# Optimization experiments

Hardware: AMD Instinct MI355X
Metric: run time of the kernel (lower is better)

## Reference

```python
import jax, jax.numpy as jnp
from jax import lax
import numpy as np

EPS = 1e-5
NEG_SLOPE = 0.2

# 4D conv via lax.conv_general_dilated (supports arbitrary spatial rank)
_DN = ('NCABXY', 'OIABXY', 'NCABXY')  # N,C + 4 spatial dims

def conv4d(x, w):
    # x: (N, Cin, S1, S2, H, W); w: (Cout, Cin, 3, 3, 3, 3); padding=1, stride=1
    return lax.conv_general_dilated(
        x, w,
        window_strides=(1, 1, 1, 1),
        padding=[(1, 1)] * 4,
        dimension_numbers=_DN,
    )

def instance_norm4d(x):
    # normalize per (n, c) over all 4 spatial dims; no affine (PyTorch default)
    mean = jnp.mean(x, axis=(2, 3, 4, 5), keepdims=True)
    var = jnp.var(x, axis=(2, 3, 4, 5), keepdims=True)
    return (x - mean) * lax.rsqrt(var + EPS)

def leaky_relu(x):
    return jnp.where(x >= 0, x, NEG_SLOPE * x)

def setup_inputs() -> dict:
    key = jax.random.key(0)
    k0, k1, k2 = jax.random.split(key, 3)
    image = jax.random.normal(k0, (1, 16, 8, 16, 64, 64), dtype=jnp.float32)
    # He-ish init scale for kernel 3^4
    w1 = jax.random.normal(k1, (32, 16, 3, 3, 3, 3), dtype=jnp.float32) * 0.03
    w2 = jax.random.normal(k2, (32, 32, 3, 3, 3, 3), dtype=jnp.float32) * 0.02
    return {"image": image, "w1": w1, "w2": w2}

def reference(image, w1, w2):
    x = leaky_relu(instance_norm4d(conv4d(image, w1)))
    x = leaky_relu(instance_norm4d(conv4d(x, w2)))
    return x
```

## Files before the change

kernel.cpp:

```cpp
#include <hip/hip_runtime.h>

#define D1 8
#define D2 16
#define HH 64
#define WW 64
#define SPATIAL (D1*D2*HH*WW)
#define EPS 1e-5f
#define NEG 0.2f

typedef unsigned short u16;
typedef __attribute__((ext_vector_type(8))) short s16x8;
typedef __attribute__((ext_vector_type(8))) unsigned short u16x8;
typedef __attribute__((ext_vector_type(4))) unsigned short u16x4;
typedef __attribute__((ext_vector_type(4))) float f32x4;

__device__ __forceinline__ u16 f2bf(float f) {
    unsigned int u = __builtin_bit_cast(unsigned int, f);
    return (u16)((u + 0x7FFFu + ((u >> 16) & 1u)) >> 16);
}
__device__ __forceinline__ float bf2f(u16 u) {
    unsigned int v = ((unsigned int)u) << 16;
    return __builtin_bit_cast(float, v);
}
__device__ __forceinline__ float leaky(float x) {
    return x >= 0.f ? x : NEG * x;
}

__device__ __forceinline__ void decode_block(int flat, int& a, int& b, int& h0) {
    int xcd  = flat & 7;
    int slot = flat >> 3;
    int ht   = slot & 7;
    int b0   = (slot >> 3) & 1;
    a        = (slot >> 4) & 7;
    b        = xcd * 2 + b0;
    h0       = ht * 8;
}

__global__ __launch_bounds__(256)
void prep(const float* __restrict__ img, const float* __restrict__ w1,
          const float* __restrict__ w2, u16* __restrict__ imgT,
          u16* __restrict__ w1t, u16* __restrict__ w2t, float* __restrict__ st)
{
    const int bid = blockIdx.x;
    const int tid = threadIdx.x;
    if (bid < 2048) {
        int p = bid * 256 + tid;
        u16 r[16];
        #pragma unroll
        for (int c = 0; c < 16; ++c)
            r[c] = f2bf(img[(size_t)c * SPATIAL + p]);
        u16x8 lo, hi;
        #pragma unroll
        for (int j = 0; j < 8; ++j) { lo[j] = r[j]; hi[j] = r[8 + j]; }
        u16x8* dst = (u16x8*)(imgT + (size_t)p * 16);
        dst[0] = lo;
        dst[1] = hi;
    } else if (bid < 2264) {
        int i = (bid - 2048) * 256 + tid;
        if (i >= 55296) return;
        int k    = i & 31;
        int co   = (i >> 5) & 31;
        int grp  = (i >> 10) & 1;
        int rest = i >> 11;
        int dh   = rest % 3;
        int p    = rest / 3;
        int da = p / 3, db = p % 3;
        float v = 0.f;
        if (grp == 0) {
            int dw = k >> 4, ci = k & 15;
            v = w1[((((co * 16 + ci) * 3 + da) * 3 + db) * 3 + dh) * 3 + dw];
        } else if (k < 16) {
            v = w1[((((co * 16 + k) * 3 + da) * 3 + db) * 3 + dh) * 3 + 2];
        }
        w1t[i] = f2bf(v);
    } else if (bid < 2588) {
        int i = (bid - 2264) * 256 + tid;
        if (i >= 82944) return;
        int ci = i & 31;
        int co = (i >> 5) & 31;
        int t  = (i >> 10) % 9;
        int p  = (i >> 10) / 9;
        int da = p / 3, db = p % 3, dh = t / 3, dw = t % 3;
        w2t[i] = f2bf(w2[((((co * 32 + ci) * 3 + da) * 3 + db) * 3 + dh) * 3 + dw]);
    } else {
        if (tid < 128) st[tid] = 0.f;
    }
}

__global__ __launch_bounds__(256, 3)
void conv1_mfma(const u16* __restrict__ xT, const u16* __restrict__ w1t,
                u16* __restrict__ y1, float* __restrict__ st1)
{
    __shared__ __align__(16) u16 lds[660 * 24];
    __shared__ float sred[64];

    const int tid = threadIdx.x;
    int a, b, h0;
    decode_block(blockIdx.x, a, b, h0);
    const int lane = tid & 63;
    const int wv   = tid >> 6;
    const int kq   = lane >> 4;
    const int m    = lane & 15;
    const int wseg = wv << 4;

    unsigned pm = 0;
    #pragma unroll
    for (int p = 0; p < 9; ++p) {
        int ap = a + p / 3 - 1, bp = b + p % 3 - 1;
        if (ap >= 0 && ap < D1 && bp >= 0 && bp < D2) pm |= 1u << p;
    }

    const int p0 = tid >> 1, g = tid & 1;
    unsigned vmask = 0;
    int goff[6];
    #pragma unroll
    for (int k = 0; k < 6; ++k) {
        int pos = p0 + 128 * k;
        int row = pos / 66, col = pos - row * 66;
        int h = h0 - 1 + row, w = col - 1;
        bool v = (pos < 660) && col >= 1 && col <= 64 && h >= 0 && h < HH;
        goff[k] = v ? (h * WW + w) * 16 + g * 8 : 0;
        vmask |= (unsigned)v << k;
    }
    const int lbase = p0 * 24 + g * 8;

    for (int e = tid; e < 660; e += 256) {
        int row = e / 66, col = e - row * 66;
        int h = h0 - 1 + row;
        if (col == 0 || col == 65 || h < 0 || h >= HH) {
            u16x8 z = (u16x8)0;
            *(u16x8*)&lds[e * 24]     = z;
            *(u16x8*)&lds[e * 24 + 8] = z;
        }
    }

    f32x4 acc[8][2];
    #pragma unroll
    for (int i = 0; i < 8; ++i)
        #pragma unroll
        for (int nt = 0; nt < 2; ++nt)
            acc[i][nt] = (f32x4)0.f;

    int p = 0;
    while (!((pm >> p) & 1)) ++p;

    u16x8 pf[6];
    {
        int ap = a + p / 3 - 1, bp = b + p % 3 - 1;
        const u16* src = xT + (size_t)(ap * D2 + bp) * (HH * WW * 16);
        #pragma unroll
        for (int k = 0; k < 6; ++k)
            if ((vmask >> k) & 1) pf[k] = *(const u16x8*)(src + goff[k]);
    }

    while (p < 9) {
        int pn = p + 1;
        while (pn < 9 && !((pm >> pn) & 1)) ++pn;

        #pragma unroll
        for (int k = 0; k < 6; ++k)
            if ((vmask >> k) & 1) *(u16x8*)&lds[lbase + k * 3072] = pf[k];
        __syncthreads();

        const u16* srcn = nullptr;
        if (pn < 9)
            srcn = xT + (size_t)((a + pn / 3 - 1) * D2 + (b + pn % 3 - 1))
                      * (HH * WW * 16);

        const u16* wbase = w1t + p * 6144;
        #pragma unroll
        for (int grp = 0; grp < 2; ++grp) {
            s16x8 bf[3][2];
            #pragma unroll
            for (int dh = 0; dh < 3; ++dh) {
                const u16* wb = wbase + (dh * 2 + grp) * 1024;
                bf[dh][0] = *(const s16x8*)(wb + m * 32 + kq * 8);
                bf[dh][1] = *(const s16x8*)(wb + (m + 16) * 32 + kq * 8);
            }
            const int cshift = (grp == 0) ? (kq >> 1) : 2;
            const int ebase  = (kq & 1) * 8;
            #pragma unroll
            for (int x = 0; x < 10; ++x) {
                int pos = x * 66 + wseg + m + cshift;
                s16x8 af = *(const s16x8*)&lds[pos * 24 + ebase];
                #pragma unroll
                for (int dh = 0; dh < 3; ++dh) {
                    int i = x - dh;
                    if (i >= 0 && i < 8) {
                        acc[i][0] = __builtin_amdgcn_mfma_f32_16x16x32_bf16(af, bf[dh][0], acc[i][0], 0, 0, 0);
                        acc[i][1] = __builtin_amdgcn_mfma_f32_16x16x32_bf16(af, bf[dh][1], acc[i][1], 0, 0, 0);
                    }
                }
            }
            if (pn < 9) {
                #pragma unroll
                for (int k = grp * 3; k < grp * 3 + 3; ++k)
                    if ((vmask >> k) & 1) pf[k] = *(const u16x8*)(srcn + goff[k]);
            }
        }
        __syncthreads();
        p = pn;
    }

    if (tid < 64) sred[tid] = 0.f;
    __syncthreads();

    float s[2] = {0.f, 0.f}, s2[2] = {0.f, 0.f};
    const size_t plane_out = (size_t)(a * D2 + b) * (HH * WW);
    #pragma unroll
    for (int i = 0; i < 8; ++i) {
        int h  = h0 + i;
        int w0 = wseg + kq * 4;
        #pragma unroll
        for (int nt = 0; nt < 2; ++nt) {
            int co = m + nt * 16;
            #pragma unroll
            for (int reg = 0; reg < 4; ++reg) {
                float v = acc[i][nt][reg];
                s[nt]  += v;
                s2[nt] += v * v;
                y1[(plane_out + h * WW + (w0 + reg)) * 32 + co] = f2bf(v);
            }
        }
    }
    #pragma unroll
    for (int nt = 0; nt < 2; ++nt) {
        s[nt]  += __shfl_xor(s[nt], 16);  s[nt]  += __shfl_xor(s[nt], 32);
        s2[nt] += __shfl_xor(s2[nt], 16); s2[nt] += __shfl_xor(s2[nt], 32);
    }
    if (kq == 0) {
        atomicAdd(&sred[m * 2],            s[0]);
        atomicAdd(&sred[m * 2 + 1],        s2[0]);
        atomicAdd(&sred[(m + 16) * 2],     s[1]);
        atomicAdd(&sred[(m + 16) * 2 + 1], s2[1]);
    }
    __syncthreads();
    if (tid < 64) atomicAdd(&st1[tid], sred[tid]);
}

__global__ __launch_bounds__(256)
void norm1_kernel(u16* __restrict__ y1, const float* __restrict__ st1)
{
    const int tid = threadIdx.x;
    const int q   = tid & 3;
    const float invN = 1.f / (float)SPATIAL;
    float mean[8], scl[8];
    #pragma unroll
    for (int j = 0; j < 8; ++j) {
        int ci  = q * 8 + j;
        float mu = st1[ci * 2] * invN;
        float va = st1[ci * 2 + 1] * invN - mu * mu;
        mean[j] = mu;
        scl[j]  = rsqrtf(va + EPS);
    }
    #pragma unroll
    for (int j4 = 0; j4 < 4; ++j4) {
        size_t gidx = (size_t)blockIdx.x * 1024 + j4 * 256 + tid;
        u16x8* ptr = (u16x8*)(y1 + gidx * 8);
        u16x8 v = *ptr;
        u16x8 o;
        #pragma unroll
        for (int j = 0; j < 8; ++j)
            o[j] = f2bf(leaky((bf2f(v[j]) - mean[j]) * scl[j]));
        *ptr = o;
    }
}

__global__ __launch_bounds__(256, 3)
void conv2_mfma(const u16* __restrict__ y1, const u16* __restrict__ w2t,
                u16* __restrict__ y2, float* __restrict__ st2)
{
    __shared__ __align__(16) u16 lds[660 * 40];
    __shared__ float sred[64];

    const int tid = threadIdx.x;
    int a, b, h0;
    decode_block(blockIdx.x, a, b, h0);
    const int lane = tid & 63;
    const int wv   = tid >> 6;
    const int kq   = lane >> 4;
    const int m    = lane & 15;
    const int wseg = wv << 4;

    unsigned pm = 0;
    #pragma unroll
    for (int p = 0; p < 9; ++p) {
        int ap = a + p / 3 - 1, bp = b + p % 3 - 1;
        if (ap >= 0 && ap < D1 && bp >= 0 && bp < D2) pm |= 1u << p;
    }

    const int p0 = tid >> 2, q = tid & 3;
    unsigned vmask = 0;
    int goff[11];
    #pragma unroll
    for (int k = 0; k < 11; ++k) {
        int pos = p0 + 64 * k;
        int row = pos / 66, col = pos - row * 66;
        int h = h0 - 1 + row, w = col - 1;
        bool v = (pos < 660) && col >= 1 && col <= 64 && h >= 0 && h < HH;
        goff[k] = v ? (h * WW + w) * 32 + q * 8 : 0;
        vmask |= (unsigned)v << k;
    }
    const int lbase = p0 * 40 + q * 8;

    for (int e = tid; e < 660; e += 256) {
        int row = e / 66, col = e - row * 66;
        int h = h0 - 1 + row;
        if (col == 0 || col == 65 || h < 0 || h >= HH) {
            u16x8 z = (u16x8)0;
            #pragma unroll
            for (int gg = 0; gg < 4; ++gg)
                *(u16x8*)&lds[e * 40 + gg * 8] = z;
        }
    }

    f32x4 acc[8][2];
    #pragma unroll
    for (int i = 0; i < 8; ++i)
        #pragma unroll
        for (int nt = 0; nt < 2; ++nt)
            acc[i][nt] = (f32x4)0.f;

    int p = 0;
    while (!((pm >> p) & 1)) ++p;

    u16x8 pf[11];
    {
        int ap = a + p / 3 - 1, bp = b + p % 3 - 1;
        const u16* src = y1 + (size_t)(ap * D2 + bp) * (HH * WW * 32);
        #pragma unroll
        for (int k = 0; k < 11; ++k)
            if ((vmask >> k) & 1) pf[k] = *(const u16x8*)(src + goff[k]);
    }

    while (p < 9) {
        int pn = p + 1;
        while (pn < 9 && !((pm >> pn) & 1)) ++pn;

        #pragma unroll
        for (int k = 0; k < 11; ++k)
            if ((vmask >> k) & 1) *(u16x8*)&lds[lbase + k * 2560] = pf[k];
        __syncthreads();

        const u16* srcn = nullptr;
        if (pn < 9)
            srcn = y1 + (size_t)((a + pn / 3 - 1) * D2 + (b + pn % 3 - 1))
                      * (HH * WW * 32);

        const u16* wbase = w2t + p * 9216;
        #pragma unroll
        for (int dw = 0; dw < 3; ++dw) {
            s16x8 bf[3][2];
            #pragma unroll
            for (int dh = 0; dh < 3; ++dh) {
                const u16* wb = wbase + (dh * 3 + dw) * 1024;
                bf[dh][0] = *(const s16x8*)(wb + m * 32 + kq * 8);
                bf[dh][1] = *(const s16x8*)(wb + (m + 16) * 32 + kq * 8);
            }
            #pragma unroll
            for (int x = 0; x < 10; ++x) {
                int pos = x * 66 + wseg + dw + m;
                s16x8 af = *(const s16x8*)&lds[pos * 40 + kq * 8];
                #pragma unroll
                for (int dh = 0; dh < 3; ++dh) {
                    int i = x - dh;
                    if (i >= 0 && i < 8) {
                        acc[i][0] = __builtin_amdgcn_mfma_f32_16x16x32_bf16(af, bf[dh][0], acc[i][0], 0, 0, 0);
                        acc[i][1] = __builtin_amdgcn_mfma_f32_16x16x32_bf16(af, bf[dh][1], acc[i][1], 0, 0, 0);
                    }
                }
            }
            if (pn < 9) {
                const int k0 = dw * 4;
                const int k1 = (dw == 2) ? 11 : (k0 + 4);
                #pragma unroll
                for (int k = k0; k < k1; ++k)
                    if ((vmask >> k) & 1) pf[k] = *(const u16x8*)(srcn + goff[k]);
            }
        }
        __syncthreads();
        p = pn;
    }

    if (tid < 64) sred[tid] = 0.f;
    __syncthreads();

    float s[2] = {0.f, 0.f}, s2[2] = {0.f, 0.f};
    #pragma unroll
    for (int i = 0; i < 8; ++i) {
        int h  = h0 + i;
        int w0 = wseg + kq * 4;
        #pragma unroll
        for (int nt = 0; nt < 2; ++nt) {
            int co = m + nt * 16;
            u16x4 pk;
            #pragma unroll
            for (int reg = 0; reg < 4; ++reg) {
                float v = acc[i][nt][reg];
                s[nt]  += v;
                s2[nt] += v * v;
                pk[reg] = f2bf(v);
            }
            size_t off = ((size_t)(co * D1 + a) * D2 + b) * (HH * WW) + h * WW + w0;
            *(u16x4*)(y2 + off) = pk;
        }
    }
    #pragma unroll
    for (int nt = 0; nt < 2; ++nt) {
        s[nt]  += __shfl_xor(s[nt], 16);  s[nt]  += __shfl_xor(s[nt], 32);
        s2[nt] += __shfl_xor(s2[nt], 16); s2[nt] += __shfl_xor(s2[nt], 32);
    }
    if (kq == 0) {
        atomicAdd(&sred[m * 2],            s[0]);
        atomicAdd(&sred[m * 2 + 1],        s2[0]);
        atomicAdd(&sred[(m + 16) * 2],     s[1]);
        atomicAdd(&sred[(m + 16) * 2 + 1], s2[1]);
    }
    __syncthreads();
    if (tid < 64) atomicAdd(&st2[tid], sred[tid]);
}

__global__ __launch_bounds__(256)
void norm2_kernel(const u16* __restrict__ y2, const float* __restrict__ st2,
                  float* __restrict__ out)
{
    size_t i4 = (size_t)blockIdx.x * 256 + threadIdx.x;
    int c = (int)(i4 >> 17);
    const float invN = 1.f / (float)SPATIAL;
    float mu = st2[c * 2] * invN;
    float va = st2[c * 2 + 1] * invN - mu * mu;
    float sc = rsqrtf(va + EPS);
    u16x4 v = *(const u16x4*)(y2 + i4 * 4);
    float4 o;
    o.x = leaky((bf2f(v[0]) - mu) * sc);
    o.y = leaky((bf2f(v[1]) - mu) * sc);
    o.z = leaky((bf2f(v[2]) - mu) * sc);
    o.w = leaky((bf2f(v[3]) - mu) * sc);
    *(float4*)(out + i4 * 4) = o;
}

extern "C" void kernel_launch(void* const* d_in, const int* in_sizes, int n_in,
                              void* d_out, int out_size, void* d_ws, size_t ws_size,
                              hipStream_t stream)
{
    const float* image = (const float*)d_in[0];
    const float* w1    = (const float*)d_in[1];
    const float* w2    = (const float*)d_in[2];
    float* out = (float*)d_out;

    u16*   imgT = (u16*)d_ws;
    u16*   y1   = (u16*)((char*)d_ws + 33554432);
    u16*   y2   = imgT;
    float* st   = (float*)((char*)d_ws + 67108864);
    float* st1  = st;
    float* st2  = st + 64;

    u16* w1t = (u16*)((char*)d_out + 66832384);
    u16* w2t = (u16*)((char*)d_out + 66942976);

    prep<<<2589, 256, 0, stream>>>(image, w1, w2, imgT, w1t, w2t, st);

    conv1_mfma<<<1024, 256, 0, stream>>>(imgT, w1t, y1, st1);
    norm1_kernel<<<2048, 256, 0, stream>>>(y1, st1);
    conv2_mfma<<<1024, 256, 0, stream>>>(y1, w2t, y2, st2);
    norm2_kernel<<<16384, 256, 0, stream>>>(y2, st2, out);
}
```

Before: 265.9 us.

## Halve conv output tile to 8x32 and double grid for higher occupancy

Both MFMA conv kernels now compute an 8-row by 32-column output tile instead of 8x64. The four waves form a 2x2 arrangement, each computing 4 rows by 16 columns, so accumulator and prefetch registers shrink, LDS halo tiles shrink, launch bounds rise to 5 blocks per CU, and the grid doubles to 2048 blocks. The goal is more concurrent waves and better latency hiding. In exchange the halo overhead per output grows (6 rows loaded per 4 computed instead of 10 per 8, plus extra column halo), which means more LDS reads and global loads per MFMA.

```diff
diff --git a/kernel.cpp b/kernel.cpp
--- a/kernel.cpp
+++ b/kernel.cpp
@@ -26,14 +26,17 @@
     return x >= 0.f ? x : NEG * x;
 }
 
-__device__ __forceinline__ void decode_block(int flat, int& a, int& b, int& h0) {
+__device__ __forceinline__ void decode_block(int flat, int& a, int& b,
+                                             int& h0, int& w0) {
     int xcd  = flat & 7;
     int slot = flat >> 3;
     int ht   = slot & 7;
-    int b0   = (slot >> 3) & 1;
-    a        = (slot >> 4) & 7;
+    int wt   = (slot >> 3) & 1;
+    int b0   = (slot >> 4) & 1;
+    a        = (slot >> 5) & 7;
     b        = xcd * 2 + b0;
     h0       = ht * 8;
+    w0       = wt * 32;
 }
 
 __global__ __launch_bounds__(256)
@@ -87,21 +90,22 @@
     }
 }
 
-__global__ __launch_bounds__(256, 3)
+__global__ __launch_bounds__(256, 5)
 void conv1_mfma(const u16* __restrict__ xT, const u16* __restrict__ w1t,
                 u16* __restrict__ y1, float* __restrict__ st1)
 {
-    __shared__ __align__(16) u16 lds[660 * 24];
+    __shared__ __align__(16) u16 lds[340 * 24];
     __shared__ float sred[64];
 
     const int tid = threadIdx.x;
-    int a, b, h0;
-    decode_block(blockIdx.x, a, b, h0);
+    int a, b, h0, w0;
+    decode_block(blockIdx.x, a, b, h0, w0);
     const int lane = tid & 63;
     const int wv   = tid >> 6;
     const int kq   = lane >> 4;
     const int m    = lane & 15;
-    const int wseg = wv << 4;
+    const int wsl  = (wv & 1) << 4;
+    const int r0   = (wv >> 1) << 2;
 
     unsigned pm = 0;
     #pragma unroll
@@ -112,31 +116,31 @@
 
     const int p0 = tid >> 1, g = tid & 1;
     unsigned vmask = 0;
-    int goff[6];
-    #pragma unroll
-    for (int k = 0; k < 6; ++k) {
+    int goff[3];
+    #pragma unroll
+    for (int k = 0; k < 3; ++k) {
         int pos = p0 + 128 * k;
-        int row = pos / 66, col = pos - row * 66;
-        int h = h0 - 1 + row, w = col - 1;
-        bool v = (pos < 660) && col >= 1 && col <= 64 && h >= 0 && h < HH;
+        int row = pos / 34, col = pos - row * 34;
+        int h = h0 - 1 + row, w = w0 + col - 1;
+        bool v = (pos < 340) && w >= 0 && w < WW && h >= 0 && h < HH;
         goff[k] = v ? (h * WW + w) * 16 + g * 8 : 0;
         vmask |= (unsigned)v << k;
     }
     const int lbase = p0 * 24 + g * 8;
 
-    for (int e = tid; e < 660; e += 256) {
-        int row = e / 66, col = e - row * 66;
-        int h = h0 - 1 + row;
-        if (col == 0 || col == 65 || h < 0 || h >= HH) {
+    for (int e = tid; e < 340; e += 256) {
+        int row = e / 34, col = e - row * 34;
+        int h = h0 - 1 + row, w = w0 + col - 1;
+        if (w < 0 || w >= WW || h < 0 || h >= HH) {
             u16x8 z = (u16x8)0;
             *(u16x8*)&lds[e * 24]     = z;
             *(u16x8*)&lds[e * 24 + 8] = z;
         }
     }
 
-    f32x4 acc[8][2];
-    #pragma unroll
-    for (int i = 0; i < 8; ++i)
+    f32x4 acc[4][2];
+    #pragma unroll
+    for (int i = 0; i < 4; ++i)
         #pragma unroll
         for (int nt = 0; nt < 2; ++nt)
             acc[i][nt] = (f32x4)0.f;
@@ -144,12 +148,12 @@
     int p = 0;
     while (!((pm >> p) & 1)) ++p;
 
-    u16x8 pf[6];
+    u16x8 pf[3];
     {
         int ap = a + p / 3 - 1, bp = b + p % 3 - 1;
         const u16* src = xT + (size_t)(ap * D2 + bp) * (HH * WW * 16);
         #pragma unroll
-        for (int k = 0; k < 6; ++k)
+        for (int k = 0; k < 3; ++k)
             if ((vmask >> k) & 1) pf[k] = *(const u16x8*)(src + goff[k]);
     }
 
@@ -158,7 +162,7 @@
         while (pn < 9 && !((pm >> pn) & 1)) ++pn;
 
         #pragma unroll
-        for (int k = 0; k < 6; ++k)
+        for (int k = 0; k < 3; ++k)
             if ((vmask >> k) & 1) *(u16x8*)&lds[lbase + k * 3072] = pf[k];
         __syncthreads();
 
@@ -180,21 +184,22 @@
             const int cshift = (grp == 0) ? (kq >> 1) : 2;
             const int ebase  = (kq & 1) * 8;
             #pragma unroll
-            for (int x = 0; x < 10; ++x) {
-                int pos = x * 66 + wseg + m + cshift;
+            for (int xi = 0; xi < 6; ++xi) {
+                int pos = (r0 + xi) * 34 + wsl + m + cshift;
                 s16x8 af = *(const s16x8*)&lds[pos * 24 + ebase];
                 #pragma unroll
                 for (int dh = 0; dh < 3; ++dh) {
-                    int i = x - dh;
-                    if (i >= 0 && i < 8) {
+                    int i = xi - dh;
+                    if (i >= 0 && i < 4) {
                         acc[i][0] = __builtin_amdgcn_mfma_f32_16x16x32_bf16(af, bf[dh][0], acc[i][0], 0, 0, 0);
                         acc[i][1] = __builtin_amdgcn_mfma_f32_16x16x32_bf16(af, bf[dh][1], acc[i][1], 0, 0, 0);
                     }
                 }
             }
             if (pn < 9) {
+                const int k0 = grp * 1, k1 = grp ? 3 : 1;
                 #pragma unroll
-                for (int k = grp * 3; k < grp * 3 + 3; ++k)
+                for (int k = k0; k < k1; ++k)
                     if ((vmask >> k) & 1) pf[k] = *(const u16x8*)(srcn + goff[k]);
             }
         }
@@ -208,9 +213,9 @@
     float s[2] = {0.f, 0.f}, s2[2] = {0.f, 0.f};
     const size_t plane_out = (size_t)(a * D2 + b) * (HH * WW);
     #pragma unroll
-    for (int i = 0; i < 8; ++i) {
-        int h  = h0 + i;
-        int w0 = wseg + kq * 4;
+    for (int i = 0; i < 4; ++i) {
+        int h  = h0 + r0 + i;
+        int w  = w0 + wsl + kq * 4;
         #pragma unroll
         for (int nt = 0; nt < 2; ++nt) {
             int co = m + nt * 16;
@@ -219,7 +224,7 @@
                 float v = acc[i][nt][reg];
                 s[nt]  += v;
                 s2[nt] += v * v;
-                y1[(plane_out + h * WW + (w0 + reg)) * 32 + co] = f2bf(v);
+                y1[(plane_out + h * WW + (w + reg)) * 32 + co] = f2bf(v);
             }
         }
     }
@@ -266,21 +271,22 @@
     }
 }
 
-__global__ __launch_bounds__(256, 3)
+__global__ __launch_bounds__(256, 5)
 void conv2_mfma(const u16* __restrict__ y1, const u16* __restrict__ w2t,
                 u16* __restrict__ y2, float* __restrict__ st2)
 {
-    __shared__ __align__(16) u16 lds[660 * 40];
+    __shared__ __align__(16) u16 lds[340 * 40];
     __shared__ float sred[64];
 
     const int tid = threadIdx.x;
-    int a, b, h0;
-    decode_block(blockIdx.x, a, b, h0);
+    int a, b, h0, w0;
+    decode_block(blockIdx.x, a, b, h0, w0);
     const int lane = tid & 63;
     const int wv   = tid >> 6;
     const int kq   = lane >> 4;
     const int m    = lane & 15;
-    const int wseg = wv << 4;
+    const int wsl  = (wv & 1) << 4;
+    const int r0   = (wv >> 1) << 2;
 
     unsigned pm = 0;
     #pragma unroll
@@ -291,22 +297,22 @@
 
     const int p0 = tid >> 2, q = tid & 3;
     unsigned vmask = 0;
-    int goff[11];
-    #pragma unroll
-    for (int k = 0; k < 11; ++k) {
+    int goff[6];
+    #pragma unroll
+    for (int k = 0; k < 6; ++k) {
         int pos = p0 + 64 * k;
-        int row = pos / 66, col = pos - row * 66;
-        int h = h0 - 1 + row, w = col - 1;
-        bool v = (pos < 660) && col >= 1 && col <= 64 && h >= 0 && h < HH;
+        int row = pos / 34, col = pos - row * 34;
+        int h = h0 - 1 + row, w = w0 + col - 1;
+        bool v = (pos < 340) && w >= 0 && w < WW && h >= 0 && h < HH;
         goff[k] = v ? (h * WW + w) * 32 + q * 8 : 0;
         vmask |= (unsigned)v << k;
     }
     const int lbase = p0 * 40 + q * 8;
 
-    for (int e = tid; e < 660; e += 256) {
-        int row = e / 66, col = e - row * 66;
-        int h = h0 - 1 + row;
-        if (col == 0 || col == 65 || h < 0 || h >= HH) {
+    for (int e = tid; e < 340; e += 256) {
+        int row = e / 34, col = e - row * 34;
+        int h = h0 - 1 + row, w = w0 + col - 1;
+        if (w < 0 || w >= WW || h < 0 || h >= HH) {
             u16x8 z = (u16x8)0;
             #pragma unroll
             for (int gg = 0; gg < 4; ++gg)
@@ -314,9 +320,9 @@
         }
     }
 
-    f32x4 acc[8][2];
-    #pragma unroll
-    for (int i = 0; i < 8; ++i)
+    f32x4 acc[4][2];
+    #pragma unroll
+    for (int i = 0; i < 4; ++i)
         #pragma unroll
         for (int nt = 0; nt < 2; ++nt)
             acc[i][nt] = (f32x4)0.f;
@@ -324,12 +330,12 @@
     int p = 0;
     while (!((pm >> p) & 1)) ++p;
 
-    u16x8 pf[11];
+    u16x8 pf[6];
     {
         int ap = a + p / 3 - 1, bp = b + p % 3 - 1;
         const u16* src = y1 + (size_t)(ap * D2 + bp) * (HH * WW * 32);
         #pragma unroll
-        for (int k = 0; k < 11; ++k)
+        for (int k = 0; k < 6; ++k)
             if ((vmask >> k) & 1) pf[k] = *(const u16x8*)(src + goff[k]);
     }
 
@@ -338,7 +344,7 @@
         while (pn < 9 && !((pm >> pn) & 1)) ++pn;
 
         #pragma unroll
-        for (int k = 0; k < 11; ++k)
+        for (int k = 0; k < 6; ++k)
             if ((vmask >> k) & 1) *(u16x8*)&lds[lbase + k * 2560] = pf[k];
         __syncthreads();
 
@@ -358,23 +364,21 @@
                 bf[dh][1] = *(const s16x8*)(wb + (m + 16) * 32 + kq * 8);
             }
             #pragma unroll
-            for (int x = 0; x < 10; ++x) {
-                int pos = x * 66 + wseg + dw + m;
+            for (int xi = 0; xi < 6; ++xi) {
+                int pos = (r0 + xi) * 34 + wsl + dw + m;
                 s16x8 af = *(const s16x8*)&lds[pos * 40 + kq * 8];
                 #pragma unroll
                 for (int dh = 0; dh < 3; ++dh) {
-                    int i = x - dh;
-                    if (i >= 0 && i < 8) {
+                    int i = xi - dh;
+                    if (i >= 0 && i < 4) {
                         acc[i][0] = __builtin_amdgcn_mfma_f32_16x16x32_bf16(af, bf[dh][0], acc[i][0], 0, 0, 0);
                         acc[i][1] = __builtin_amdgcn_mfma_f32_16x16x32_bf16(af, bf[dh][1], acc[i][1], 0, 0, 0);
                     }
                 }
             }
             if (pn < 9) {
-                const int k0 = dw * 4;
-                const int k1 = (dw == 2) ? 11 : (k0 + 4);
                 #pragma unroll
-                for (int k = k0; k < k1; ++k)
+                for (int k = dw * 2; k < dw * 2 + 2; ++k)
                     if ((vmask >> k) & 1) pf[k] = *(const u16x8*)(srcn + goff[k]);
             }
         }
@@ -387,9 +391,9 @@
 
     float s[2] = {0.f, 0.f}, s2[2] = {0.f, 0.f};
     #pragma unroll
-    for (int i = 0; i < 8; ++i) {
-        int h  = h0 + i;
-        int w0 = wseg + kq * 4;
+    for (int i = 0; i < 4; ++i) {
+        int h = h0 + r0 + i;
+        int w = w0 + wsl + kq * 4;
         #pragma unroll
         for (int nt = 0; nt < 2; ++nt) {
             int co = m + nt * 16;
@@ -401,7 +405,7 @@
                 s2[nt] += v * v;
                 pk[reg] = f2bf(v);
             }
-            size_t off = ((size_t)(co * D1 + a) * D2 + b) * (HH * WW) + h * WW + w0;
+            size_t off = ((size_t)(co * D1 + a) * D2 + b) * (HH * WW) + h * WW + w;
             *(u16x4*)(y2 + off) = pk;
         }
     }
@@ -460,8 +464,8 @@
 
     prep<<<2589, 256, 0, stream>>>(image, w1, w2, imgT, w1t, w2t, st);
 
-    conv1_mfma<<<1024, 256, 0, stream>>>(imgT, w1t, y1, st1);
+    conv1_mfma<<<2048, 256, 0, stream>>>(imgT, w1t, y1, st1);
     norm1_kernel<<<2048, 256, 0, stream>>>(y1, st1);
-    conv2_mfma<<<1024, 256, 0, stream>>>(y1, w2t, y2, st2);
+    conv2_mfma<<<2048, 256, 0, stream>>>(y1, w2t, y2, st2);
     norm2_kernel<<<16384, 256, 0, stream>>>(y2, st2, out);
 }
```

Result: slower. 505.6 us (+90.2%).
